# Optimization experiments

Hardware: AMD Instinct MI355X
Metric: run time of the kernel (lower is better)

## Reference

```python
import jax, jax.numpy as jnp
import numpy as np

B, F, T, H, K = 512, 64, 64, 512, 4  # batch, in_feat, timesteps, hidden, num cells (air0,bed0,air1,bed1)


def setup_inputs() -> dict:
    key = jax.random.key(0)
    ks = jax.random.split(key, 10)
    s = 1.0 / np.sqrt(H)
    u = lambda k, shape: jax.random.uniform(k, shape, jnp.float32, -s, s)
    return {
        "data": jax.random.normal(ks[0], (B, F, T), jnp.float32),
        "init": jax.random.normal(ks[1], (B, H), jnp.float32),
        # stacked params for the 4 branches in order [air0, bed0, air1, bed1]
        "fc_in_W": u(ks[2], (K, H, F)),
        "fc_in_b": u(ks[3], (K, H)),
        "Wih": u(ks[4], (K, 3 * H, H)),   # torch GRUCell weight_ih, gate order r,z,n
        "Whh": u(ks[5], (K, 3 * H, H)),
        "bih": u(ks[6], (K, 3 * H)),
        "bhh": u(ks[7], (K, 3 * H)),
        "fc_out_W": u(ks[8], (2, H)),     # [air, bed] output heads (Linear(512,1))
        "fc_out_b": u(ks[9], (2,)),
    }


def reference(data, init, fc_in_W, fc_in_b, Wih, Whh, bih, bhh, fc_out_W, fc_out_b):
    # Input projections (Linear + ReLU; Dropout is identity in eval): [T, K, B, H]
    proj = jax.nn.relu(jnp.einsum('bft,kof->tkbo', data, fc_in_W) + fc_in_b[None, :, None, :])
    # branches 2,3 (air1, bed1) consume the sequence reversed (data[:, :, 63-i])
    x_seq = jnp.concatenate([proj[:, :2], proj[::-1, 2:]], axis=1)  # [T, K, B, H]

    h0 = jnp.broadcast_to(init[None], (K,) + init.shape)  # all 4 cells start from init

    def step(h, x):  # h, x: [K, B, H]
        gi = jnp.einsum('kbi,koi->kbo', x, Wih) + bih[:, None, :]
        gh = jnp.einsum('kbi,koi->kbo', h, Whh) + bhh[:, None, :]
        ir, iz, inn = jnp.split(gi, 3, axis=-1)
        hr, hz, hn = jnp.split(gh, 3, axis=-1)
        r = jax.nn.sigmoid(ir + hr)
        z = jax.nn.sigmoid(iz + hz)
        n = jnp.tanh(inn + r * hn)
        h_new = (1.0 - z) * n + z * h
        return h_new, h_new

    _, hs = jax.lax.scan(step, h0, x_seq)  # [T, K, B, H]

    # output i (1..64) combines fwd hidden[i] with bwd hidden[65-i] -> reverse bwd stack
    air = hs[:, 0] + hs[::-1, 2]  # [T, B, H]
    bed = hs[:, 1] + hs[::-1, 3]
    air_out = (jnp.einsum('tbh,h->tb', air, fc_out_W[0]) + fc_out_b[0]).T  # [B, T]
    bed_out = (jnp.einsum('tbh,h->tb', bed, fc_out_W[1]) + fc_out_b[1]).T
    return air_out, bed_out
```

## Files before the change

### kernel.cpp

```cpp
#include <hip/hip_runtime.h>
#include <hip/hip_bf16.h>

typedef __hip_bfloat16 bf16;
typedef __attribute__((ext_vector_type(8))) short short8;
typedef __attribute__((ext_vector_type(4))) float f32x4;

#define Hdim 512
#define Bdim 512
#define Tdim 64
#define Fdim 64
#define NC   4

__device__ __forceinline__ float sigmoidf_(float x){ return 1.f/(1.f + __expf(-x)); }
__device__ __forceinline__ float tanhf_(float x){
  float t = __expf(-2.f*fabsf(x));
  float r = (1.f - t)/(1.f + t);
  return copysignf(r, x);
}
__device__ __forceinline__ float bf2f_(short u){
  return __uint_as_float(((unsigned)(unsigned short)u) << 16);
}
__device__ __forceinline__ short f2bf_(float f){
  bf16 b = (bf16)f;
  return *(short*)&b;
}

__global__ __launch_bounds__(256) void pack_kernel(const float* __restrict__ src,
                                                   bf16* __restrict__ dst, int n){
  int idx = (blockIdx.x*256 + threadIdx.x)*4;
  if (idx < n){
    float4 v = *(const float4*)(src + idx);
    dst[idx+0] = (bf16)v.x;
    dst[idx+1] = (bf16)v.y;
    dst[idx+2] = (bf16)v.z;
    dst[idx+3] = (bf16)v.w;
  }
}

__global__ __launch_bounds__(256) void transpose_kernel(const float* __restrict__ data,
                                                        bf16* __restrict__ dataT){
  __shared__ bf16 tile[64*65];
  int b = blockIdx.x;
  int tid = threadIdx.x;
  for (int i = 0; i < 16; ++i){
    int idx = tid + i*256;
    int f = idx >> 6, t = idx & 63;
    tile[f*65 + t] = (bf16)data[(b*64 + f)*64 + t];
  }
  __syncthreads();
  for (int i = 0; i < 16; ++i){
    int idx = tid + i*256;
    int t = idx >> 6, f = idx & 63;
    dataT[(t*Bdim + b)*64 + f] = tile[f*65 + t];
  }
}

__global__ __launch_bounds__(256) void init_kernel(const float* __restrict__ init_h,
                            bf16* __restrict__ h_b1, unsigned* __restrict__ flags){
  int idx = blockIdx.x*256 + threadIdx.x;
  int k = idx >> 18;
  int rem = idx & 262143;
  int bg = rem >> 9;
  int o  = rem & 511;
  int dst = ((k*2 + (bg >> 8))*16 + (o >> 5))*8192 + (bg & 255)*32 + (o & 31);
  h_b1[dst] = (bf16)init_h[rem];
  if (idx < 512) flags[idx] = 0u;
}

__global__ __launch_bounds__(256) void proj_kernel(const bf16* __restrict__ dataT,
    const bf16* __restrict__ fc_in_W, const float* __restrict__ fc_in_b,
    bf16* __restrict__ x_seq){
  __shared__ short ldsA[64*72];
  __shared__ short ldsW[128*72];
  int blk = blockIdx.x;
  int s  = blk >> 7;
  int k  = (blk >> 5) & 3;
  int bt = (blk >> 2) & 7;
  int on = blk & 3;
  int tid = threadIdx.x;
  int lane = tid & 63, wid = tid >> 6;
  int quad = lane >> 4, l16 = lane & 15;
  int src_t = (k < 2) ? s : (Tdim - 1 - s);

  const short* Ag = (const short*)(dataT + (src_t*Bdim + bt*64)*Fdim);
  #pragma unroll
  for (int i = 0; i < 2; ++i){
    int c = tid + i*256; int r = c >> 3, off = c & 7;
    *(int4*)(&ldsA[r*72 + off*8]) = *(const int4*)(&Ag[r*64 + off*8]);
  }
  const short* Wg = (const short*)(fc_in_W + (k*Hdim + on*128)*Fdim);
  #pragma unroll
  for (int i = 0; i < 4; ++i){
    int c = tid + i*256; int r = c >> 3, off = c & 7;
    *(int4*)(&ldsW[r*72 + off*8]) = *(const int4*)(&Wg[r*64 + off*8]);
  }
  __syncthreads();

  f32x4 acc[2][4];
  #pragma unroll
  for (int nt=0; nt<2; ++nt)
    #pragma unroll
    for (int rb=0; rb<4; ++rb) acc[nt][rb] = (f32x4){0.f,0.f,0.f,0.f};

  #pragma unroll
  for (int kk = 0; kk < 2; ++kk){
    int io = kk*32 + quad*8;
    short8 a[4];
    #pragma unroll
    for (int rb=0; rb<4; ++rb) a[rb] = *(const short8*)(&ldsA[(rb*16+l16)*72 + io]);
    #pragma unroll
    for (int nt=0; nt<2; ++nt){
      short8 bw = *(const short8*)(&ldsW[(wid*32 + nt*16 + l16)*72 + io]);
      #pragma unroll
      for (int rb=0; rb<4; ++rb)
        acc[nt][rb] = __builtin_amdgcn_mfma_f32_16x16x32_bf16(a[rb], bw, acc[nt][rb], 0,0,0);
    }
  }

  #pragma unroll
  for (int nt=0; nt<2; ++nt){
    int o = on*128 + wid*32 + nt*16 + l16;
    float bias = fc_in_b[k*Hdim + o];
    #pragma unroll
    for (int rb=0; rb<4; ++rb){
      #pragma unroll
      for (int reg=0; reg<4; ++reg){
        int b = bt*64 + rb*16 + quad*4 + reg;
        float v = acc[nt][rb][reg] + bias;
        v = v > 0.f ? v : 0.f;
        x_seq[((size_t)(s*NC + k)*Bdim + b)*Hdim + o] = (bf16)v;
      }
    }
  }
}

__global__ __launch_bounds__(512) void rnn_kernel(
    const bf16* __restrict__ x_seq, const float* __restrict__ init_h,
    bf16* __restrict__ h_b0, bf16* __restrict__ h_b1,
    const float* __restrict__ Wih, const float* __restrict__ Whh,
    const float* __restrict__ bih, const float* __restrict__ bhh,
    const float* __restrict__ fc_out_W,
    bf16* __restrict__ gi, float* __restrict__ part,
    unsigned* __restrict__ flags, unsigned* __restrict__ xslot)
{
  __shared__ short wlds[3*2*16*512];
  __shared__ int sslot;

  int tid = threadIdx.x;
  int lane = tid & 63, wid = tid >> 6;
  int quad = lane >> 4, l16 = lane & 15;

  unsigned xcc;
  asm volatile("s_getreg_b32 %0, hwreg(HW_REG_XCC_ID)" : "=s"(xcc));
  xcc &= 7u;
  if (tid == 0)
    sslot = (int)__hip_atomic_fetch_add(&xslot[xcc*32], 1u,
                __ATOMIC_RELAXED, __HIP_MEMORY_SCOPE_WORKGROUP);
  __syncthreads();
  int grp = (int)xcc;
  int k   = grp >> 1;
  int bt  = grp & 1;
  int slot = sslot & 31;
  int producer = (slot < 16);
  int j    = slot & 15;
  int obase = j*32;
  int rot  = slot & 15;
  unsigned* gflags = flags + grp*32;

  const float* Wsrc = producer ? Wih : Whh;
  for (int i = tid; i < 3*2*16*64; i += 512){
    int plane = i >> 11;
    int rem   = i & 2047;
    int nt    = rem >> 10;
    int rem2  = rem & 1023;
    int kc    = rem2 >> 6;
    int ln    = rem2 & 63;
    int ll16  = ln & 15, lq = ln >> 4;
    const float* srcp = Wsrc +
        ((size_t)(k*3 + plane)*Hdim + obase + nt*16 + ll16)*Hdim + kc*32 + lq*8;
    float4 f0 = *(const float4*)srcp;
    float4 f1 = *(const float4*)(srcp + 4);
    short8 pk;
    pk[0]=f2bf_(f0.x); pk[1]=f2bf_(f0.y); pk[2]=f2bf_(f0.z); pk[3]=f2bf_(f0.w);
    pk[4]=f2bf_(f1.x); pk[5]=f2bf_(f1.y); pk[6]=f2bf_(f1.z); pk[7]=f2bf_(f1.w);
    *(int4*)(&wlds[i*8]) = *(int4*)&pk;
  }

  #define GEMM32X(ABASE) do {                                                   \
    const short* ap0_ = (ABASE) + (wid*32 + l16)*Hdim + quad*8;                 \
    const short* ap1_ = ap0_ + 16*Hdim;                                         \
    short8 ab_[4][2];                                                           \
    _Pragma("unroll")                                                           \
    for (int d=0; d<4; ++d){                                                    \
      int c_ = (d + rot) & 15;                                                  \
      ab_[d][0] = *(const short8*)(ap0_ + c_*32);                               \
      ab_[d][1] = *(const short8*)(ap1_ + c_*32);                               \
    }                                                                           \
    short8 bb_[2][6];                                                           \
    _Pragma("unroll")                                                           \
    for (int p=0; p<6; ++p)                                                     \
      bb_[0][p] = *(const short8*)(&wlds[((p*16 + rot)<<9) + (lane<<3)]);       \
    _Pragma("unroll")                                                           \
    for (int kc=0; kc<16; ++kc){                                                \
      short8 a0_ = ab_[kc&3][0], a1_ = ab_[kc&3][1];                            \
      if (kc < 12){                                                             \
        int c_ = (kc + 4 + rot) & 15;                                           \
        ab_[kc&3][0] = *(const short8*)(ap0_ + c_*32);                          \
        ab_[kc&3][1] = *(const short8*)(ap1_ + c_*32);                          \
      }                                                                         \
      if (kc < 15){                                                             \
        int c_ = (kc + 1 + rot) & 15;                                           \
        _Pragma("unroll")                                                       \
        for (int p=0; p<6; ++p)                                                 \
          bb_[(kc+1)&1][p] = *(const short8*)(&wlds[((p*16 + c_)<<9) + (lane<<3)]); \
      }                                                                         \
      _Pragma("unroll")                                                         \
      for (int g=0; g<3; ++g){                                                  \
        _Pragma("unroll")                                                       \
        for (int nt=0; nt<2; ++nt){                                             \
          short8 bw_ = bb_[kc&1][g*2+nt];                                       \
          acc[g][nt][0] = __builtin_amdgcn_mfma_f32_16x16x32_bf16(a0_, bw_, acc[g][nt][0], 0,0,0); \
          acc[g][nt][1] = __builtin_amdgcn_mfma_f32_16x16x32_bf16(a1_, bw_, acc[g][nt][1], 0,0,0); \
        }                                                                       \
      }                                                                         \
    }                                                                           \
  } while(0)

  #define GEMM32H(HCB) do {                                                     \
    const short* hp0_ = (HCB) + (wid*32 + l16)*32 + quad*8;                     \
    const short* hp1_ = hp0_ + 16*32;                                           \
    short8 ab_[4][2];                                                           \
    _Pragma("unroll")                                                           \
    for (int d=0; d<4; ++d){                                                    \
      int c_ = (d + rot) & 15;                                                  \
      ab_[d][0] = *(const short8*)(hp0_ + c_*8192);                             \
      ab_[d][1] = *(const short8*)(hp1_ + c_*8192);                             \
    }                                                                           \
    short8 bb_[2][6];                                                           \
    _Pragma("unroll")                                                           \
    for (int p=0; p<6; ++p)                                                     \
      bb_[0][p] = *(const short8*)(&wlds[((p*16 + rot)<<9) + (lane<<3)]);       \
    _Pragma("unroll")                                                           \
    for (int kc=0; kc<16; ++kc){                                                \
      short8 a0_ = ab_[kc&3][0], a1_ = ab_[kc&3][1];                            \
      if (kc < 12){                                                             \
        int c_ = (kc + 4 + rot) & 15;                                           \
        ab_[kc&3][0] = *(const short8*)(hp0_ + c_*8192);                        \
        ab_[kc&3][1] = *(const short8*)(hp1_ + c_*8192);                        \
      }                                                                         \
      if (kc < 15){                                                             \
        int c_ = (kc + 1 + rot) & 15;                                           \
        _Pragma("unroll")                                                       \
        for (int p=0; p<6; ++p)                                                 \
          bb_[(kc+1)&1][p] = *(const short8*)(&wlds[((p*16 + c_)<<9) + (lane<<3)]); \
      }                                                                         \
      _Pragma("unroll")                                                         \
      for (int g=0; g<3; ++g){                                                  \
        _Pragma("unroll")                                                       \
        for (int nt=0; nt<2; ++nt){                                             \
          short8 bw_ = bb_[kc&1][g*2+nt];                                       \
          acc[g][nt][0] = __builtin_amdgcn_mfma_f32_16x16x32_bf16(a0_, bw_, acc[g][nt][0], 0,0,0); \
          acc[g][nt][1] = __builtin_amdgcn_mfma_f32_16x16x32_bf16(a1_, bw_, acc[g][nt][1], 0,0,0); \
        }                                                                       \
      }                                                                         \
    }                                                                           \
  } while(0)

  #define WAITFLAGS(PTHR, CTHR) do {                                            \
    if (wid == 0){                                                              \
      unsigned thr_ = (lane < 16) ? (unsigned)(PTHR) : (unsigned)(CTHR);        \
      int g_ = 0;                                                               \
      for (;;){                                                                 \
        unsigned v_ = 0xFFFFFFFFu;                                              \
        if (lane < 32)                                                          \
          v_ = __hip_atomic_load(&gflags[lane], __ATOMIC_RELAXED,               \
                                 __HIP_MEMORY_SCOPE_AGENT);                     \
        if (__ballot(v_ >= thr_) == ~0ull) break;                               \
        __builtin_amdgcn_s_sleep(2);                                            \
        if (++g_ > 2000000) break;                                              \
      }                                                                         \
    }                                                                           \
    __syncthreads();                                                            \
  } while(0)

  if (producer){
    __syncthreads();
    for (int s = 0; s < 64; ++s){
      f32x4 acc[3][2][2];
      #pragma unroll
      for (int g=0; g<3; ++g)
        #pragma unroll
        for (int nt=0; nt<2; ++nt){
          acc[g][nt][0] = (f32x4){0.f,0.f,0.f,0.f};
          acc[g][nt][1] = (f32x4){0.f,0.f,0.f,0.f};
        }
      if (s >= 2) WAITFLAGS(0u, (unsigned)(s-1));
      const short* x_base = (const short*)(x_seq + ((size_t)(s*NC + k)*Bdim + bt*256)*Hdim);
      GEMM32X(x_base);
      bf16* gb = gi + ((size_t)(((s&1)*8 + grp)*16 + j))*24576;
      #pragma unroll
      for (int g=0; g<3; ++g){
        #pragma unroll
        for (int nt=0; nt<2; ++nt){
          short8 pk;
          #pragma unroll
          for (int rb=0; rb<2; ++rb)
            #pragma unroll
            for (int reg=0; reg<4; ++reg)
              pk[rb*4+reg] = f2bf_(acc[g][nt][rb][reg]);
          *(int4*)(gb + ((g*2+nt)*512 + wid*64 + lane)*8) = *(int4*)&pk;
        }
      }
      __syncthreads();
      if (tid == 0)
        __hip_atomic_fetch_add(&gflags[slot], 1u,
                               __ATOMIC_RELAXED, __HIP_MEMORY_SCOPE_AGENT);
    }
  } else {
    int o0 = obase + l16, o1 = o0 + 16;
    float br0  = bih[k*3*Hdim + o0] + bhh[k*3*Hdim + o0];
    float br1  = bih[k*3*Hdim + o1] + bhh[k*3*Hdim + o1];
    float bz0  = bih[k*3*Hdim + Hdim + o0] + bhh[k*3*Hdim + Hdim + o0];
    float bz1  = bih[k*3*Hdim + Hdim + o1] + bhh[k*3*Hdim + Hdim + o1];
    float bnx0 = bih[k*3*Hdim + 2*Hdim + o0];
    float bnx1 = bih[k*3*Hdim + 2*Hdim + o1];
    float bnh0 = bhh[k*3*Hdim + 2*Hdim + o0];
    float bnh1 = bhh[k*3*Hdim + 2*Hdim + o1];
    float wout0 = fc_out_W[(k & 1)*Hdim + o0];
    float wout1 = fc_out_W[(k & 1)*Hdim + o1];

    float hk[2][2][4];
    #pragma unroll
    for (int nt=0; nt<2; ++nt)
      #pragma unroll
      for (int rb=0; rb<2; ++rb)
        #pragma unroll
        for (int reg=0; reg<4; ++reg)
          hk[nt][rb][reg] =
            init_h[(bt*256 + wid*32 + rb*16 + quad*4 + reg)*Hdim + obase + nt*16 + l16];

    __syncthreads();

    const int hgrp = (k*2 + bt)*16;

    for (int s = 0; s < 64; ++s){
      const bf16* h_in  = (s & 1) ? h_b0 : h_b1;
      bf16*       h_out = (s & 1) ? h_b1 : h_b0;

      f32x4 acc[3][2][2];
      #pragma unroll
      for (int g=0; g<3; ++g)
        #pragma unroll
        for (int nt=0; nt<2; ++nt){
          acc[g][nt][0] = (f32x4){0.f,0.f,0.f,0.f};
          acc[g][nt][1] = (f32x4){0.f,0.f,0.f,0.f};
        }

      WAITFLAGS((unsigned)(s+1), (unsigned)s);

      const bf16* gb = gi + ((size_t)(((s&1)*8 + grp)*16 + j))*24576;
      short8 gv[6];
      #pragma unroll
      for (int p=0; p<6; ++p){
        int4 t = *(const int4*)(gb + (p*512 + wid*64 + lane)*8);
        gv[p] = *(short8*)&t;
      }

      const short* h_cb = (const short*)h_in + (size_t)hgrp*8192;
      GEMM32H(h_cb);

      int tmap = (k < 2) ? s : (Tdim - 1 - s);
      bf16* hob = h_out + (size_t)(hgrp + j)*8192;
      #pragma unroll
      for (int rb = 0; rb < 2; ++rb){
        #pragma unroll
        for (int reg = 0; reg < 4; ++reg){
          int bl = wid*32 + rb*16 + quad*4 + reg;
          float v = 0.f;
          #pragma unroll
          for (int nt = 0; nt < 2; ++nt){
            float gir = bf2f_(gv[0*2+nt][rb*4+reg]);
            float giz = bf2f_(gv[1*2+nt][rb*4+reg]);
            float gin = bf2f_(gv[2*2+nt][rb*4+reg]);
            float br  = nt ? br1 : br0,  bz = nt ? bz1 : bz0;
            float bnx = nt ? bnx1 : bnx0, bnh = nt ? bnh1 : bnh0;
            float r = sigmoidf_(gir + acc[0][nt][rb][reg] + br);
            float z = sigmoidf_(giz + acc[1][nt][rb][reg] + bz);
            float n = tanhf_(gin + bnx + r*(acc[2][nt][rb][reg] + bnh));
            float hn = (1.f - z)*n + z*hk[nt][rb][reg];
            hk[nt][rb][reg] = hn;
            hob[bl*32 + nt*16 + l16] = (bf16)hn;
            v += hn * (nt ? wout1 : wout0);
          }
          v += __shfl_xor(v, 1, 64);
          v += __shfl_xor(v, 2, 64);
          v += __shfl_xor(v, 4, 64);
          v += __shfl_xor(v, 8, 64);
          if (l16 == 0)
            __builtin_nontemporal_store(v,
              &part[((size_t)(k*Tdim + tmap)*16 + j)*Bdim + bt*256 + bl]);
        }
      }

      __syncthreads();
      if (tid == 0)
        __hip_atomic_fetch_add(&gflags[slot], 1u,
                               __ATOMIC_RELAXED, __HIP_MEMORY_SCOPE_AGENT);
    }
  }
  #undef GEMM32X
  #undef GEMM32H
  #undef WAITFLAGS
}

__global__ __launch_bounds__(256) void finalize_kernel(const float* __restrict__ part,
                                const float* __restrict__ fc_out_b, float* __restrict__ out){
  int idx = blockIdx.x*256 + threadIdx.x;
  int head = idx >> 15;
  int b = (idx >> 6) & 511;
  int t = idx & 63;
  float v = fc_out_b[head];
  #pragma unroll
  for (int kk = 0; kk < 2; ++kk){
    const float* p = part + (size_t)((head + kk*2)*Tdim + t)*16*Bdim + b;
    #pragma unroll
    for (int jj = 0; jj < 16; ++jj)
      v += p[jj*Bdim];
  }
  out[idx] = v;
}

extern "C" void kernel_launch(void* const* d_in, const int* in_sizes, int n_in,
                              void* d_out, int out_size, void* d_ws, size_t ws_size,
                              hipStream_t stream){
  (void)in_sizes; (void)n_in; (void)out_size; (void)ws_size;
  const float* data     = (const float*)d_in[0];
  const float* init_h   = (const float*)d_in[1];
  const float* fc_in_W  = (const float*)d_in[2];
  const float* fc_in_b  = (const float*)d_in[3];
  const float* Wih      = (const float*)d_in[4];
  const float* Whh      = (const float*)d_in[5];
  const float* bih      = (const float*)d_in[6];
  const float* bhh      = (const float*)d_in[7];
  const float* fc_out_W = (const float*)d_in[8];
  const float* fc_out_b = (const float*)d_in[9];
  float* out = (float*)d_out;

  char* ws = (char*)d_ws;
  bf16*  x_seq   = (bf16*)ws;
  bf16*  h_b0    = (bf16*)(ws + 134217728);
  bf16*  h_b1    = (bf16*)(ws + 136314880);
  bf16*  gi      = (bf16*)(ws + 138412032);
  bf16*  dataT   = (bf16*)(ws + 138412032);
  float* part    = (float*)(ws + 150994944);
  bf16*  fcW_bf  = (bf16*)(ws + 159383552);
  unsigned* flags= (unsigned*)(ws + 159645696);
  unsigned* xslot= (unsigned*)(ws + 159646720);

  const int nFW = NC*Hdim*Fdim;
  hipLaunchKernelGGL(pack_kernel, dim3(nFW/1024), dim3(256), 0, stream, fc_in_W, fcW_bf, nFW);
  hipLaunchKernelGGL(init_kernel, dim3(4096), dim3(256), 0, stream, init_h, h_b1, flags);
  hipLaunchKernelGGL(transpose_kernel, dim3(512), dim3(256), 0, stream, data, dataT);
  hipLaunchKernelGGL(proj_kernel, dim3(8192), dim3(256), 0, stream, dataT, fcW_bf, fc_in_b, x_seq);
  hipLaunchKernelGGL(rnn_kernel, dim3(256), dim3(512), 0, stream,
      x_seq, init_h, h_b0, h_b1, Wih, Whh, bih, bhh, fc_out_W, gi, part, flags, xslot);
  hipLaunchKernelGGL(finalize_kernel, dim3(256), dim3(256), 0, stream, part, fc_out_b, out);
}
```

Before: 814.3 us.

## Replace all-to-all flag barrier with per-chunk dataflow waits in GRU recurrence

Each block now waits only on the specific flags it depends on instead of ballot-waiting on all 32 group flags with a block-wide barrier. Consumers poll the 16 hidden-state chunk flags per wave and process each K-chunk as soon as its producer publishes it, in rotated order. This overlaps MFMA work with stragglers in the recurrent step. In exchange it adds per-wave polling in the inner loop, drops the deeper 4-chunk prefetch, and relies on relaxed atomics plus a compiler barrier for memory ordering.

New measurement: 903.4 us. 10.9% more time.

```diff
diff --git a/kernel.cpp b/kernel.cpp
--- a/kernel.cpp
+++ b/kernel.cpp
@@ -164,7 +164,7 @@
   int producer = (slot < 16);
   int j    = slot & 15;
   int obase = j*32;
-  int rot  = slot & 15;
+  int rot  = j;
   unsigned* gflags = flags + grp*32;
 
   const float* Wsrc = producer ? Wih : Whh;
@@ -226,61 +226,14 @@
     }                                                                           \
   } while(0)
 
-  #define GEMM32H(HCB) do {                                                     \
-    const short* hp0_ = (HCB) + (wid*32 + l16)*32 + quad*8;                     \
-    const short* hp1_ = hp0_ + 16*32;                                           \
-    short8 ab_[4][2];                                                           \
-    _Pragma("unroll")                                                           \
-    for (int d=0; d<4; ++d){                                                    \
-      int c_ = (d + rot) & 15;                                                  \
-      ab_[d][0] = *(const short8*)(hp0_ + c_*8192);                             \
-      ab_[d][1] = *(const short8*)(hp1_ + c_*8192);                             \
+  #define WAITONE(fidx, thr) do {                                               \
+    int g_ = 0;                                                                 \
+    while (__hip_atomic_load(&gflags[fidx], __ATOMIC_RELAXED,                   \
+                             __HIP_MEMORY_SCOPE_AGENT) < (unsigned)(thr)){      \
+      __builtin_amdgcn_s_sleep(1);                                              \
+      if (++g_ > 4000000) break;                                                \
     }                                                                           \
-    short8 bb_[2][6];                                                           \
-    _Pragma("unroll")                                                           \
-    for (int p=0; p<6; ++p)                                                     \
-      bb_[0][p] = *(const short8*)(&wlds[((p*16 + rot)<<9) + (lane<<3)]);       \
-    _Pragma("unroll")                                                           \
-    for (int kc=0; kc<16; ++kc){                                                \
-      short8 a0_ = ab_[kc&3][0], a1_ = ab_[kc&3][1];                            \
-      if (kc < 12){                                                             \
-        int c_ = (kc + 4 + rot) & 15;                                           \
-        ab_[kc&3][0] = *(const short8*)(hp0_ + c_*8192);                        \
-        ab_[kc&3][1] = *(const short8*)(hp1_ + c_*8192);                        \
-      }                                                                         \
-      if (kc < 15){                                                             \
-        int c_ = (kc + 1 + rot) & 15;                                           \
-        _Pragma("unroll")                                                       \
-        for (int p=0; p<6; ++p)                                                 \
-          bb_[(kc+1)&1][p] = *(const short8*)(&wlds[((p*16 + c_)<<9) + (lane<<3)]); \
-      }                                                                         \
-      _Pragma("unroll")                                                         \
-      for (int g=0; g<3; ++g){                                                  \
-        _Pragma("unroll")                                                       \
-        for (int nt=0; nt<2; ++nt){                                             \
-          short8 bw_ = bb_[kc&1][g*2+nt];                                       \
-          acc[g][nt][0] = __builtin_amdgcn_mfma_f32_16x16x32_bf16(a0_, bw_, acc[g][nt][0], 0,0,0); \
-          acc[g][nt][1] = __builtin_amdgcn_mfma_f32_16x16x32_bf16(a1_, bw_, acc[g][nt][1], 0,0,0); \
-        }                                                                       \
-      }                                                                         \
-    }                                                                           \
-  } while(0)
-
-  #define WAITFLAGS(PTHR, CTHR) do {                                            \
-    if (wid == 0){                                                              \
-      unsigned thr_ = (lane < 16) ? (unsigned)(PTHR) : (unsigned)(CTHR);        \
-      int g_ = 0;                                                               \
-      for (;;){                                                                 \
-        unsigned v_ = 0xFFFFFFFFu;                                              \
-        if (lane < 32)                                                          \
-          v_ = __hip_atomic_load(&gflags[lane], __ATOMIC_RELAXED,               \
-                                 __HIP_MEMORY_SCOPE_AGENT);                     \
-        if (__ballot(v_ >= thr_) == ~0ull) break;                               \
-        __builtin_amdgcn_s_sleep(2);                                            \
-        if (++g_ > 2000000) break;                                              \
-      }                                                                         \
-    }                                                                           \
-    __syncthreads();                                                            \
+    __asm__ __volatile__("" ::: "memory");                                      \
   } while(0)
 
   if (producer){
@@ -294,7 +247,7 @@
           acc[g][nt][0] = (f32x4){0.f,0.f,0.f,0.f};
           acc[g][nt][1] = (f32x4){0.f,0.f,0.f,0.f};
         }
-      if (s >= 2) WAITFLAGS(0u, (unsigned)(s-1));
+      if (s >= 2) WAITONE(16 + j, s - 1);
       const short* x_base = (const short*)(x_seq + ((size_t)(s*NC + k)*Bdim + bt*256)*Hdim);
       GEMM32X(x_base);
       bf16* gb = gi + ((size_t)(((s&1)*8 + grp)*16 + j))*24576;
@@ -313,7 +266,7 @@
       }
       __syncthreads();
       if (tid == 0)
-        __hip_atomic_fetch_add(&gflags[slot], 1u,
+        __hip_atomic_fetch_add(&gflags[j], 1u,
                                __ATOMIC_RELAXED, __HIP_MEMORY_SCOPE_AGENT);
     }
   } else {
@@ -343,6 +296,44 @@
 
     const int hgrp = (k*2 + bt)*16;
 
+    #define HLOADC(c, A0, A1, B) do {                                           \
+      A0 = *(const short8*)(hp0 + (size_t)(c)*8192);                            \
+      A1 = *(const short8*)(hp1 + (size_t)(c)*8192);                            \
+      _Pragma("unroll")                                                         \
+      for (int p=0; p<6; ++p)                                                   \
+        B[p] = *(const short8*)(&wlds[((p*16 + (c))<<9) + (lane<<3)]);          \
+    } while(0)
+    #define HMFMAC(A0, A1, B) do {                                              \
+      _Pragma("unroll")                                                         \
+      for (int g=0; g<3; ++g){                                                  \
+        _Pragma("unroll")                                                       \
+        for (int nt=0; nt<2; ++nt){                                             \
+          acc[g][nt][0] = __builtin_amdgcn_mfma_f32_16x16x32_bf16(A0, B[g*2+nt], acc[g][nt][0], 0,0,0); \
+          acc[g][nt][1] = __builtin_amdgcn_mfma_f32_16x16x32_bf16(A1, B[g*2+nt], acc[g][nt][1], 0,0,0); \
+        }                                                                       \
+      }                                                                         \
+    } while(0)
+    #define PICKH(cvar) do {                                                    \
+      int g_ = 0;                                                               \
+      while (!avail){                                                           \
+        unsigned v_ = 0xFFFFFFFFu;                                              \
+        if (lane < 16)                                                          \
+          v_ = __hip_atomic_load(&gflags[16 + lane], __ATOMIC_RELAXED,          \
+                                 __HIP_MEMORY_SCOPE_AGENT);                     \
+        unsigned r_ = (unsigned)__ballot(v_ >= (unsigned)s) & 0xFFFFu;          \
+        avail = r_ & ~done;                                                     \
+        if (!avail){                                                            \
+          __builtin_amdgcn_s_sleep(1);                                          \
+          if (++g_ > 4000000) avail = 0xFFFFu & ~done;                          \
+        }                                                                       \
+      }                                                                         \
+      unsigned hi_ = avail >> rot;                                              \
+      cvar = hi_ ? rot + __builtin_ctz(hi_) : __builtin_ctz(avail);             \
+      avail &= ~(1u << cvar);                                                   \
+      done  |= (1u << cvar);                                                    \
+      __asm__ __volatile__("" ::: "memory");                                    \
+    } while(0)
+
     for (int s = 0; s < 64; ++s){
       const bf16* h_in  = (s & 1) ? h_b0 : h_b1;
       bf16*       h_out = (s & 1) ? h_b1 : h_b0;
@@ -356,7 +347,7 @@
           acc[g][nt][1] = (f32x4){0.f,0.f,0.f,0.f};
         }
 
-      WAITFLAGS((unsigned)(s+1), (unsigned)s);
+      WAITONE(j, s + 1);
 
       const bf16* gb = gi + ((size_t)(((s&1)*8 + grp)*16 + j))*24576;
       short8 gv[6];
@@ -366,8 +357,26 @@
         gv[p] = *(short8*)&t;
       }
 
-      const short* h_cb = (const short*)h_in + (size_t)hgrp*8192;
-      GEMM32H(h_cb);
+      const short* hp0 = (const short*)h_in + (size_t)hgrp*8192 + (wid*32 + l16)*32 + quad*8;
+      const short* hp1 = hp0 + 16*32;
+      {
+        unsigned done = 0;
+        unsigned avail = (s == 0) ? 0xFFFFu : 0u;
+        int c;
+        short8 A0c, A1c, Bc[6], A0n, A1n, Bn[6];
+        PICKH(c);
+        HLOADC(c, A0c, A1c, Bc);
+        #pragma unroll 1
+        for (int it = 1; it < 16; ++it){
+          PICKH(c);
+          HLOADC(c, A0n, A1n, Bn);
+          HMFMAC(A0c, A1c, Bc);
+          A0c = A0n; A1c = A1n;
+          #pragma unroll
+          for (int p=0; p<6; ++p) Bc[p] = Bn[p];
+        }
+        HMFMAC(A0c, A1c, Bc);
+      }
 
       int tmap = (k < 2) ? s : (Tdim - 1 - s);
       bf16* hob = h_out + (size_t)(hgrp + j)*8192;
@@ -404,13 +413,15 @@
 
       __syncthreads();
       if (tid == 0)
-        __hip_atomic_fetch_add(&gflags[slot], 1u,
+        __hip_atomic_fetch_add(&gflags[16 + j], 1u,
                                __ATOMIC_RELAXED, __HIP_MEMORY_SCOPE_AGENT);
     }
+    #undef HLOADC
+    #undef HMFMAC
+    #undef PICKH
   }
   #undef GEMM32X
-  #undef GEMM32H
-  #undef WAITFLAGS
+  #undef WAITONE
 }
 
 __global__ __launch_bounds__(256) void finalize_kernel(const float* __restrict__ part,
```

## Loosen producer-consumer sync with triple-buffered gates and per-slot flag waits

Applied to the files above, without the earlier changes.

Producers now wait only on their matching consumer flag, not on all 32 slots of the group, and the gate buffer grows from double to triple buffering so producers can run one step further ahead. Consumers wait on all consumer flags plus only their own producer flag. They also signal completion right after writing h, before the output-head reduction, which takes that reduction off the critical path. Workspace offsets move to fit the larger gate buffer. The cost is more workspace, and correctness now depends on the narrower flag dependencies being sufficient.

After: 743.4 us (median of 2 runs). -8.7%, faster.

```diff
diff --git a/kernel.cpp b/kernel.cpp
--- a/kernel.cpp
+++ b/kernel.cpp
@@ -164,7 +164,7 @@
   int producer = (slot < 16);
   int j    = slot & 15;
   int obase = j*32;
-  int rot  = slot & 15;
+  int rot  = j;
   unsigned* gflags = flags + grp*32;
 
   const float* Wsrc = producer ? Wih : Whh;
@@ -266,23 +266,6 @@
     }                                                                           \
   } while(0)
 
-  #define WAITFLAGS(PTHR, CTHR) do {                                            \
-    if (wid == 0){                                                              \
-      unsigned thr_ = (lane < 16) ? (unsigned)(PTHR) : (unsigned)(CTHR);        \
-      int g_ = 0;                                                               \
-      for (;;){                                                                 \
-        unsigned v_ = 0xFFFFFFFFu;                                              \
-        if (lane < 32)                                                          \
-          v_ = __hip_atomic_load(&gflags[lane], __ATOMIC_RELAXED,               \
-                                 __HIP_MEMORY_SCOPE_AGENT);                     \
-        if (__ballot(v_ >= thr_) == ~0ull) break;                               \
-        __builtin_amdgcn_s_sleep(2);                                            \
-        if (++g_ > 2000000) break;                                              \
-      }                                                                         \
-    }                                                                           \
-    __syncthreads();                                                            \
-  } while(0)
-
   if (producer){
     __syncthreads();
     for (int s = 0; s < 64; ++s){
@@ -294,10 +277,20 @@
           acc[g][nt][0] = (f32x4){0.f,0.f,0.f,0.f};
           acc[g][nt][1] = (f32x4){0.f,0.f,0.f,0.f};
         }
-      if (s >= 2) WAITFLAGS(0u, (unsigned)(s-1));
+      if (s >= 3){
+        if (wid == 0){
+          int g_ = 0;
+          while (__hip_atomic_load(&gflags[16 + j], __ATOMIC_RELAXED,
+                                   __HIP_MEMORY_SCOPE_AGENT) < (unsigned)(s - 2)){
+            __builtin_amdgcn_s_sleep(1);
+            if (++g_ > 4000000) break;
+          }
+        }
+        __syncthreads();
+      }
       const short* x_base = (const short*)(x_seq + ((size_t)(s*NC + k)*Bdim + bt*256)*Hdim);
       GEMM32X(x_base);
-      bf16* gb = gi + ((size_t)(((s&1)*8 + grp)*16 + j))*24576;
+      bf16* gb = gi + ((size_t)(((s % 3)*8 + grp)*16 + j))*24576;
       #pragma unroll
       for (int g=0; g<3; ++g){
         #pragma unroll
@@ -313,7 +306,7 @@
       }
       __syncthreads();
       if (tid == 0)
-        __hip_atomic_fetch_add(&gflags[slot], 1u,
+        __hip_atomic_fetch_add(&gflags[j], 1u,
                                __ATOMIC_RELAXED, __HIP_MEMORY_SCOPE_AGENT);
     }
   } else {
@@ -356,9 +349,29 @@
           acc[g][nt][1] = (f32x4){0.f,0.f,0.f,0.f};
         }
 
-      WAITFLAGS((unsigned)(s+1), (unsigned)s);
-
-      const bf16* gb = gi + ((size_t)(((s&1)*8 + grp)*16 + j))*24576;
+      {
+        if (wid == 0){
+          int g_ = 0;
+          for (;;){
+            unsigned v_ = 0xFFFFFFFFu, thr_ = 0u;
+            if (lane < 16){
+              v_ = __hip_atomic_load(&gflags[16 + lane], __ATOMIC_RELAXED,
+                                     __HIP_MEMORY_SCOPE_AGENT);
+              thr_ = (unsigned)s;
+            } else if (lane == 16){
+              v_ = __hip_atomic_load(&gflags[j], __ATOMIC_RELAXED,
+                                     __HIP_MEMORY_SCOPE_AGENT);
+              thr_ = (unsigned)(s + 1);
+            }
+            if (__ballot(v_ >= thr_) == ~0ull) break;
+            __builtin_amdgcn_s_sleep(1);
+            if (++g_ > 4000000) break;
+          }
+        }
+        __syncthreads();
+      }
+
+      const bf16* gb = gi + ((size_t)(((s % 3)*8 + grp)*16 + j))*24576;
       short8 gv[6];
       #pragma unroll
       for (int p=0; p<6; ++p){
@@ -369,14 +382,13 @@
       const short* h_cb = (const short*)h_in + (size_t)hgrp*8192;
       GEMM32H(h_cb);
 
-      int tmap = (k < 2) ? s : (Tdim - 1 - s);
+      float hnv[2][2][4];
       bf16* hob = h_out + (size_t)(hgrp + j)*8192;
       #pragma unroll
       for (int rb = 0; rb < 2; ++rb){
         #pragma unroll
         for (int reg = 0; reg < 4; ++reg){
           int bl = wid*32 + rb*16 + quad*4 + reg;
-          float v = 0.f;
           #pragma unroll
           for (int nt = 0; nt < 2; ++nt){
             float gir = bf2f_(gv[0*2+nt][rb*4+reg]);
@@ -389,9 +401,24 @@
             float n = tanhf_(gin + bnx + r*(acc[2][nt][rb][reg] + bnh));
             float hn = (1.f - z)*n + z*hk[nt][rb][reg];
             hk[nt][rb][reg] = hn;
+            hnv[nt][rb][reg] = hn;
             hob[bl*32 + nt*16 + l16] = (bf16)hn;
-            v += hn * (nt ? wout1 : wout0);
           }
+        }
+      }
+
+      __syncthreads();
+      if (tid == 0)
+        __hip_atomic_fetch_add(&gflags[16 + j], 1u,
+                               __ATOMIC_RELAXED, __HIP_MEMORY_SCOPE_AGENT);
+
+      int tmap = (k < 2) ? s : (Tdim - 1 - s);
+      #pragma unroll
+      for (int rb = 0; rb < 2; ++rb){
+        #pragma unroll
+        for (int reg = 0; reg < 4; ++reg){
+          int bl = wid*32 + rb*16 + quad*4 + reg;
+          float v = hnv[0][rb][reg]*wout0 + hnv[1][rb][reg]*wout1;
           v += __shfl_xor(v, 1, 64);
           v += __shfl_xor(v, 2, 64);
           v += __shfl_xor(v, 4, 64);
@@ -401,16 +428,10 @@
               &part[((size_t)(k*Tdim + tmap)*16 + j)*Bdim + bt*256 + bl]);
         }
       }
-
-      __syncthreads();
-      if (tid == 0)
-        __hip_atomic_fetch_add(&gflags[slot], 1u,
-                               __ATOMIC_RELAXED, __HIP_MEMORY_SCOPE_AGENT);
     }
   }
   #undef GEMM32X
   #undef GEMM32H
-  #undef WAITFLAGS
 }
 
 __global__ __launch_bounds__(256) void finalize_kernel(const float* __restrict__ part,
@@ -452,10 +473,10 @@
   bf16*  h_b1    = (bf16*)(ws + 136314880);
   bf16*  gi      = (bf16*)(ws + 138412032);
   bf16*  dataT   = (bf16*)(ws + 138412032);
-  float* part    = (float*)(ws + 150994944);
-  bf16*  fcW_bf  = (bf16*)(ws + 159383552);
-  unsigned* flags= (unsigned*)(ws + 159645696);
-  unsigned* xslot= (unsigned*)(ws + 159646720);
+  float* part    = (float*)(ws + 157286400);
+  bf16*  fcW_bf  = (bf16*)(ws + 165675008);
+  unsigned* flags= (unsigned*)(ws + 165937152);
+  unsigned* xslot= (unsigned*)(ws + 165938176);
 
   const int nFW = NC*Hdim*Fdim;
   hipLaunchKernelGGL(pack_kernel, dim3(nFW/1024), dim3(256), 0, stream, fc_in_W, fcW_bf, nFW);
```
